# Performance work log

Measured on AMD Instinct MI355X. Metric: run time of the kernel, lower is better.

The kernel has to match this reference:

```python
import math
import jax, jax.numpy as jnp
import numpy as np

D_MODEL = 1024
N_HEAD = 16
D_K = D_MODEL // N_HEAD  # 64
D_V = D_MODEL // N_HEAD  # 64


def setup_inputs() -> dict:
    key = jax.random.key(0)
    kx, kq, kk, kv, ko = jax.random.split(key, 5)
    B, L = 4, 2048
    x = jax.random.normal(kx, (B, L, D_MODEL), dtype=jnp.float32)
    mask = jnp.zeros((B, 1, 1, L), dtype=bool)  # True = masked; all-False here
    s = 1.0 / math.sqrt(D_MODEL)
    # torch nn.Linear weights: shape (out_features, in_features), y = x @ W.T
    Wq = jax.random.normal(kq, (D_K * N_HEAD, D_MODEL), dtype=jnp.float32) * s
    Wk = jax.random.normal(kk, (D_K * N_HEAD, D_MODEL), dtype=jnp.float32) * s
    Wv = jax.random.normal(kv, (D_V * N_HEAD, D_MODEL), dtype=jnp.float32) * s
    Wo = jax.random.normal(ko, (D_MODEL, D_V * N_HEAD), dtype=jnp.float32) * s
    return {"x": x, "mask": mask, "Wq": Wq, "Wk": Wk, "Wv": Wv, "Wo": Wo}


def reference(x, mask, Wq, Wk, Wv, Wo):
    B, L, D = x.shape
    H, Dh, Dv = N_HEAD, D_K, D_V
    # projections (torch Linear: x @ W.T), then split heads -> (B,H,L,Dh)
    q = (x @ Wq.T).reshape(B, L, H, Dh).transpose(0, 2, 1, 3)
    k = (x @ Wk.T).reshape(B, L, H, Dh).transpose(0, 2, 1, 3)
    v = (x @ Wv.T).reshape(B, L, H, Dv).transpose(0, 2, 1, 3)
    scores = jnp.einsum('bhqd,bhkd->bhqk', q, k) / math.sqrt(Dh)
    scores = jnp.where(mask, -jnp.inf, scores)
    attn = jax.nn.softmax(scores, axis=-1)  # dropout p=0.0 -> identity
    out = jnp.einsum('bhqk,bhkd->bhqd', attn, v)  # (B,H,L,Dv)
    out = out.transpose(0, 2, 1, 3).reshape(B, L, H * Dv)
    return out @ Wo.T
```

## Files before the change

kernel.cpp:

```cpp
#include <hip/hip_runtime.h>

typedef __bf16 bf16_t;
typedef __bf16 bf16x4 __attribute__((ext_vector_type(4)));
typedef __bf16 bf16x8 __attribute__((ext_vector_type(8)));
typedef float f32x4 __attribute__((ext_vector_type(4)));

#define MFMA_16x16x32 __builtin_amdgcn_mfma_f32_16x16x32_bf16

#define GLD16(dst_lds, src_glb) \
  __builtin_amdgcn_global_load_lds((__attribute__((address_space(1))) void*)(void*)(src_glb), \
                                   (__attribute__((address_space(3))) void*)(dst_lds), 16, 0, 0)


__global__ void cvt_all(const float* __restrict__ x,  const float* __restrict__ wq,
                        const float* __restrict__ wk, const float* __restrict__ wv,
                        const float* __restrict__ wo,
                        bf16_t* __restrict__ xb, bf16_t* __restrict__ wqkv,
                        bf16_t* __restrict__ wob) {
    const int XN = 8 * 1024 * 1024, WN = 1024 * 1024;
    int i = (blockIdx.x * blockDim.x + threadIdx.x) * 4;
    const float* s; bf16_t* d; int off;
    if (i < XN)                { s = x;  d = xb;            off = i; }
    else if (i < XN + WN)      { s = wq; d = wqkv;          off = i - XN; }
    else if (i < XN + 2 * WN)  { s = wk; d = wqkv + WN;     off = i - XN - WN; }
    else if (i < XN + 3 * WN)  { s = wv; d = wqkv + 2 * WN; off = i - XN - 2 * WN; }
    else                       { s = wo; d = wob;           off = i - XN - 3 * WN; }
    float4 v = *(const float4*)(s + off);
    bf16x4 o;
    o[0] = (bf16_t)v.x; o[1] = (bf16_t)v.y; o[2] = (bf16_t)v.z; o[3] = (bf16_t)v.w;
    *(bf16x4*)(d + off) = o;
}

__global__ __launch_bounds__(256) void gemm_qkv(
    const bf16_t* __restrict__ A, const bf16_t* __restrict__ W,
    bf16_t* __restrict__ qo, bf16_t* __restrict__ ko, bf16_t* __restrict__ vto)
{
    constexpr int K = 1024, BK = 32;
    __shared__ bf16_t smem[16896];
    bf16_t* As = smem;
    bf16_t* Bs = smem + 4096;
    const int t = threadIdx.x;
    const int lane = t & 63, wave = t >> 6;
    const int quad = lane >> 4, l16 = lane & 15;
    const int m0 = blockIdx.x * 128, n0 = blockIdx.y * 128;
    const int wm = (wave & 1) * 64, wn = (wave >> 1) * 64;

    f32x4 acc[4][4] = {};

    const int c0 = t, c1 = t + 256;
    const int r0 = c0 >> 2, o0 = (c0 & 3) * 8;
    const int r1 = c1 >> 2, o1 = (c1 & 3) * 8;

    for (int k0 = 0; k0 < K; k0 += BK) {
        __syncthreads();
        GLD16(As + c0 * 8, A + (size_t)(m0 + r0) * K + k0 + o0);
        GLD16(As + c1 * 8, A + (size_t)(m0 + r1) * K + k0 + o1);
        GLD16(Bs + c0 * 8, W + (size_t)(n0 + r0) * K + k0 + o0);
        GLD16(Bs + c1 * 8, W + (size_t)(n0 + r1) * K + k0 + o1);
        __syncthreads();
        bf16x8 af[4], bfr[4];
#pragma unroll
        for (int i = 0; i < 4; ++i)
            af[i] = *(const bf16x8*)(As + (wm + i * 16 + l16) * BK + quad * 8);
#pragma unroll
        for (int j = 0; j < 4; ++j)
            bfr[j] = *(const bf16x8*)(Bs + (wn + j * 16 + l16) * BK + quad * 8);
#pragma unroll
        for (int i = 0; i < 4; ++i)
#pragma unroll
            for (int j = 0; j < 4; ++j)
                acc[i][j] = MFMA_16x16x32(af[i], bfr[j], acc[i][j], 0, 0, 0);
    }

    if (n0 < 2048) {
#pragma unroll
        for (int i = 0; i < 4; ++i) {
#pragma unroll
            for (int j = 0; j < 4; ++j) {
#pragma unroll
                for (int r = 0; r < 4; ++r) {
                    int row = m0 + wm + i * 16 + quad * 4 + r;
                    int col = n0 + wn + j * 16 + l16;
                    float v = acc[i][j][r];
                    int b = row >> 11, l = row & 2047;
                    int sec = col >> 10, c2 = col & 1023;
                    int h = c2 >> 6, dd = c2 & 63;
                    size_t bh = (size_t)b * 16 + h;
                    if (sec == 0) qo[(bh * 2048 + l) * 64 + dd] = (bf16_t)(v * 0.125f);
                    else          ko[(bh * 2048 + l) * 64 + dd] = (bf16_t)v;
                }
            }
        }
    } else {
        __syncthreads();
        const int hh = wave >> 1;
#pragma unroll
        for (int i = 0; i < 4; ++i) {
            int lbase = wm + (i >> 1) * 32;
            int slot0 = quad * 8 + (i & 1) * 4;
#pragma unroll
            for (int j = 0; j < 4; ++j) {
                int dd = j * 16 + l16;
                bf16x4 pk;
#pragma unroll
                for (int r = 0; r < 4; ++r) pk[r] = (bf16_t)acc[i][j][r];
                *(bf16x4*)(smem + (hh * 64 + dd) * 132 + lbase + slot0) = pk;
            }
        }
        __syncthreads();
        const int b = m0 >> 11, lb = m0 & 2047;
        const int h0 = (n0 - 2048) >> 6;
#pragma unroll
        for (int r8 = 0; r8 < 8; ++r8) {
            int c = r8 * 256 + t;
            int ch = c >> 10, cc = c & 1023;
            int dd = cc >> 4, lc = (cc & 15) * 8;
            bf16x8 vv = *(const bf16x8*)(smem + (ch * 64 + dd) * 132 + lc);
            size_t bh = (size_t)b * 16 + h0 + ch;
            *(bf16x8*)(vto + (bh * 64 + dd) * 2048 + lb + lc) = vv;
        }
    }
}

__global__ __launch_bounds__(256) void gemm_out(
    const bf16_t* __restrict__ A, const bf16_t* __restrict__ W,
    float* __restrict__ out)
{
    constexpr int K = 1024, BK = 32;
    __shared__ bf16_t As[128 * BK];
    __shared__ bf16_t Bs[128 * BK];
    const int t = threadIdx.x;
    const int lane = t & 63, wave = t >> 6;
    const int quad = lane >> 4, l16 = lane & 15;
    const int m0 = blockIdx.x * 128, n0 = blockIdx.y * 128;
    const int wm = (wave & 1) * 64, wn = (wave >> 1) * 64;

    f32x4 acc[4][4] = {};

    const int c0 = t, c1 = t + 256;
    const int r0 = c0 >> 2, o0 = (c0 & 3) * 8;
    const int r1 = c1 >> 2, o1 = (c1 & 3) * 8;

    for (int k0 = 0; k0 < K; k0 += BK) {
        __syncthreads();
        GLD16(As + c0 * 8, A + (size_t)(m0 + r0) * K + k0 + o0);
        GLD16(As + c1 * 8, A + (size_t)(m0 + r1) * K + k0 + o1);
        GLD16(Bs + c0 * 8, W + (size_t)(n0 + r0) * K + k0 + o0);
        GLD16(Bs + c1 * 8, W + (size_t)(n0 + r1) * K + k0 + o1);
        __syncthreads();
        bf16x8 af[4], bfr[4];
#pragma unroll
        for (int i = 0; i < 4; ++i)
            af[i] = *(const bf16x8*)(As + (wm + i * 16 + l16) * BK + quad * 8);
#pragma unroll
        for (int j = 0; j < 4; ++j)
            bfr[j] = *(const bf16x8*)(Bs + (wn + j * 16 + l16) * BK + quad * 8);
#pragma unroll
        for (int i = 0; i < 4; ++i)
#pragma unroll
            for (int j = 0; j < 4; ++j)
                acc[i][j] = MFMA_16x16x32(af[i], bfr[j], acc[i][j], 0, 0, 0);
    }

#pragma unroll
    for (int i = 0; i < 4; ++i)
#pragma unroll
        for (int j = 0; j < 4; ++j)
#pragma unroll
            for (int r = 0; r < 4; ++r) {
                int row = m0 + wm + i * 16 + quad * 4 + r;
                int col = n0 + wn + j * 16 + l16;
                out[(size_t)row * 1024 + col] = acc[i][j][r];
            }
}

__global__ __launch_bounds__(256, 2) void attn(
    const bf16_t* __restrict__ q, const bf16_t* __restrict__ k,
    const bf16_t* __restrict__ vt, bf16_t* __restrict__ ho)
{
    constexpr int L = 2048, DH = 64;
    const int bid = blockIdx.x;
    const int bh = bid & 63, qblk = bid >> 6;
    const bf16_t* Q   = q  + (size_t)bh * L * DH;
    const bf16_t* Kg  = k  + (size_t)bh * L * DH;
    const bf16_t* VTg = vt + (size_t)bh * L * DH;
    const int t = threadIdx.x, lane = t & 63, wave = t >> 6;
    const int quad = lane >> 4, l16 = lane & 15;
    const int qrow0 = qblk * 256 + wave * 64;

    __shared__ bf16_t Ks[4096];
    __shared__ bf16_t Vs[4096];

    const int c0 = t, c1 = t + 256;
    const bf16_t* ks0 = Kg  + (size_t)((c0 >> 2) & 63) * DH + (c0 >> 8) * 32 + (c0 & 3) * 8;
    const bf16_t* ks1 = Kg  + (size_t)((c1 >> 2) & 63) * DH + (c1 >> 8) * 32 + (c1 & 3) * 8;
    const bf16_t* vs0 = VTg + (size_t)((c0 >> 2) & 63) * L  + (c0 >> 8) * 32 + (c0 & 3) * 8;
    const bf16_t* vs1 = VTg + (size_t)((c1 >> 2) & 63) * L  + (c1 >> 8) * 32 + (c1 & 3) * 8;

    bf16x8 bq[4][2];
#pragma unroll
    for (int s4 = 0; s4 < 4; ++s4) {
        bq[s4][0] = *(const bf16x8*)(Q + (size_t)(qrow0 + s4 * 16 + l16) * DH + quad * 8);
        bq[s4][1] = *(const bf16x8*)(Q + (size_t)(qrow0 + s4 * 16 + l16) * DH + 32 + quad * 8);
    }

    f32x4 o[4][4] = {};
    float ls[4] = {};

    for (int kc = 0; kc < L; kc += 64) {
        __syncthreads();
        GLD16(Ks + c0 * 8, ks0 + (size_t)kc * DH);
        GLD16(Ks + c1 * 8, ks1 + (size_t)kc * DH);
        GLD16(Vs + c0 * 8, vs0 + kc);
        GLD16(Vs + c1 * 8, vs1 + kc);
        __syncthreads();

#pragma unroll
        for (int h = 0; h < 2; ++h) {
            bf16x8 ak[2][2];
#pragma unroll
            for (int ss = 0; ss < 2; ++ss) {
                ak[ss][0] = *(const bf16x8*)(Ks + ((h * 2 + ss) * 16 + l16) * 32 + quad * 8);
                ak[ss][1] = *(const bf16x8*)(Ks + 2048 + ((h * 2 + ss) * 16 + l16) * 32 + quad * 8);
            }
            f32x4 st[4][2];
#pragma unroll
            for (int q4 = 0; q4 < 4; ++q4)
#pragma unroll
                for (int ss = 0; ss < 2; ++ss) {
                    f32x4 z = {};
                    z = MFMA_16x16x32(ak[ss][0], bq[q4][0], z, 0, 0, 0);
                    st[q4][ss] = MFMA_16x16x32(ak[ss][1], bq[q4][1], z, 0, 0, 0);
                }
            bf16x8 p[4];
#pragma unroll
            for (int q4 = 0; q4 < 4; ++q4)
#pragma unroll
                for (int r = 0; r < 4; ++r) {
                    float e0 = __expf(st[q4][0][r]);
                    float e1 = __expf(st[q4][1][r]);
                    p[q4][r]     = (bf16_t)e0;
                    p[q4][4 + r] = (bf16_t)e1;
                    ls[q4] += e0 + e1;
                }
#pragma unroll
            for (int tt = 0; tt < 4; ++tt) {
                bf16x8 av = *(const bf16x8*)(Vs + h * 2048 + (tt * 16 + l16) * 32 + quad * 8);
#pragma unroll
                for (int q4 = 0; q4 < 4; ++q4)
                    o[q4][tt] = MFMA_16x16x32(av, p[q4], o[q4][tt], 0, 0, 0);
            }
        }
    }

    const int b = bh >> 4, hd = bh & 15;
#pragma unroll
    for (int q4 = 0; q4 < 4; ++q4) {
        float s = ls[q4];
        s += __shfl_xor(s, 16);
        s += __shfl_xor(s, 32);
        const float inv = 1.0f / s;
        const int tok = b * 2048 + qrow0 + q4 * 16 + l16;
#pragma unroll
        for (int tt = 0; tt < 4; ++tt) {
            bf16x4 ov;
#pragma unroll
            for (int r = 0; r < 4; ++r) ov[r] = (bf16_t)(o[q4][tt][r] * inv);
            *(bf16x4*)(ho + (size_t)tok * 1024 + hd * 64 + tt * 16 + quad * 4) = ov;
        }
    }
}

extern "C" void kernel_launch(void* const* d_in, const int* in_sizes, int n_in,
                              void* d_out, int out_size, void* d_ws, size_t ws_size,
                              hipStream_t stream) {
    const float* x  = (const float*)d_in[0];
    const float* Wq = (const float*)d_in[2];
    const float* Wk = (const float*)d_in[3];
    const float* Wv = (const float*)d_in[4];
    const float* Wo = (const float*)d_in[5];
    float* out = (float*)d_out;

    bf16_t* ws   = (bf16_t*)d_ws;
    bf16_t* xb   = ws;
    bf16_t* wqkv = xb   + (size_t)8192 * 1024;
    bf16_t* wob  = wqkv + (size_t)3072 * 1024;
    bf16_t* qb   = wob  + (size_t)1024 * 1024;
    bf16_t* kb   = qb   + (size_t)8192 * 1024;
    bf16_t* vtb  = kb   + (size_t)8192 * 1024;
    bf16_t* hob  = vtb  + (size_t)8192 * 1024;

    cvt_all<<<12288, 256, 0, stream>>>(x, Wq, Wk, Wv, Wo, xb, wqkv, wob);
    gemm_qkv<<<dim3(64, 24), 256, 0, stream>>>(xb, wqkv, qb, kb, vtb);
    attn<<<512, 256, 0, stream>>>(qb, kb, vtb, hob);
    gemm_out<<<dim3(64, 8), 256, 0, stream>>>(hob, wob, out);
}
```

Baseline: 258.0 us.

## Widen GEMM K-tiles with XOR-swizzled LDS and retile attention for more blocks

Both GEMMs now stage a 64-wide K slice per iteration, XOR-swizzling the LDS layout to avoid bank conflicts, which halves the number of barrier pairs. The attention kernel processes 128 keys per chunk with swizzled K/V tiles, gives each wave 32 query rows instead of 64, and launches twice as many blocks with a higher occupancy hint. The softmax scale now folds log2(e) into the Q scale so exp2f can be used. The cost is fewer query rows per wave, so K/V data loaded into LDS is reused less per block.

```diff
diff --git a/kernel.cpp b/kernel.cpp
--- a/kernel.cpp
+++ b/kernel.cpp
@@ -11,6 +11,7 @@
   __builtin_amdgcn_global_load_lds((__attribute__((address_space(1))) void*)(void*)(src_glb), \
                                    (__attribute__((address_space(3))) void*)(dst_lds), 16, 0, 0)
 
+#define QSCALE 0.18033688011112042f
 
 __global__ void cvt_all(const float* __restrict__ x,  const float* __restrict__ wq,
                         const float* __restrict__ wk, const float* __restrict__ wv,
@@ -35,10 +36,10 @@
     const bf16_t* __restrict__ A, const bf16_t* __restrict__ W,
     bf16_t* __restrict__ qo, bf16_t* __restrict__ ko, bf16_t* __restrict__ vto)
 {
-    constexpr int K = 1024, BK = 32;
+    constexpr int K = 1024, BK = 64;
     __shared__ bf16_t smem[16896];
     bf16_t* As = smem;
-    bf16_t* Bs = smem + 4096;
+    bf16_t* Bs = smem + 8192;
     const int t = threadIdx.x;
     const int lane = t & 63, wave = t >> 6;
     const int quad = lane >> 4, l16 = lane & 15;
@@ -47,29 +48,39 @@
 
     f32x4 acc[4][4] = {};
 
-    const int c0 = t, c1 = t + 256;
-    const int r0 = c0 >> 2, o0 = (c0 & 3) * 8;
-    const int r1 = c1 >> 2, o1 = (c1 & 3) * 8;
+    int goff[4];
+#pragma unroll
+    for (int m = 0; m < 4; ++m) {
+        int c = t + m * 256;
+        int row = c >> 3;
+        goff[m] = row * K + (((c & 7) ^ (row & 7)) * 8);
+    }
 
     for (int k0 = 0; k0 < K; k0 += BK) {
         __syncthreads();
-        GLD16(As + c0 * 8, A + (size_t)(m0 + r0) * K + k0 + o0);
-        GLD16(As + c1 * 8, A + (size_t)(m0 + r1) * K + k0 + o1);
-        GLD16(Bs + c0 * 8, W + (size_t)(n0 + r0) * K + k0 + o0);
-        GLD16(Bs + c1 * 8, W + (size_t)(n0 + r1) * K + k0 + o1);
-        __syncthreads();
-        bf16x8 af[4], bfr[4];
-#pragma unroll
-        for (int i = 0; i < 4; ++i)
-            af[i] = *(const bf16x8*)(As + (wm + i * 16 + l16) * BK + quad * 8);
-#pragma unroll
-        for (int j = 0; j < 4; ++j)
-            bfr[j] = *(const bf16x8*)(Bs + (wn + j * 16 + l16) * BK + quad * 8);
-#pragma unroll
-        for (int i = 0; i < 4; ++i)
+#pragma unroll
+        for (int m = 0; m < 4; ++m) {
+            int c8 = (t + m * 256) * 8;
+            GLD16(As + c8, A + (size_t)m0 * K + k0 + goff[m]);
+            GLD16(Bs + c8, W + (size_t)n0 * K + k0 + goff[m]);
+        }
+        __syncthreads();
+#pragma unroll
+        for (int half = 0; half < 2; ++half) {
+            const int sw = (((half * 4 + quad) ^ (l16 & 7)) * 8);
+            bf16x8 af[4], bfr[4];
+#pragma unroll
+            for (int i = 0; i < 4; ++i)
+                af[i] = *(const bf16x8*)(As + (wm + i * 16 + l16) * 64 + sw);
 #pragma unroll
             for (int j = 0; j < 4; ++j)
-                acc[i][j] = MFMA_16x16x32(af[i], bfr[j], acc[i][j], 0, 0, 0);
+                bfr[j] = *(const bf16x8*)(Bs + (wn + j * 16 + l16) * 64 + sw);
+#pragma unroll
+            for (int i = 0; i < 4; ++i)
+#pragma unroll
+                for (int j = 0; j < 4; ++j)
+                    acc[i][j] = MFMA_16x16x32(af[i], bfr[j], acc[i][j], 0, 0, 0);
+        }
     }
 
     if (n0 < 2048) {
@@ -86,7 +97,7 @@
                     int sec = col >> 10, c2 = col & 1023;
                     int h = c2 >> 6, dd = c2 & 63;
                     size_t bh = (size_t)b * 16 + h;
-                    if (sec == 0) qo[(bh * 2048 + l) * 64 + dd] = (bf16_t)(v * 0.125f);
+                    if (sec == 0) qo[(bh * 2048 + l) * 64 + dd] = (bf16_t)(v * QSCALE);
                     else          ko[(bh * 2048 + l) * 64 + dd] = (bf16_t)v;
                 }
             }
@@ -126,9 +137,10 @@
     const bf16_t* __restrict__ A, const bf16_t* __restrict__ W,
     float* __restrict__ out)
 {
-    constexpr int K = 1024, BK = 32;
-    __shared__ bf16_t As[128 * BK];
-    __shared__ bf16_t Bs[128 * BK];
+    constexpr int K = 1024, BK = 64;
+    __shared__ bf16_t smem[16384];
+    bf16_t* As = smem;
+    bf16_t* Bs = smem + 8192;
     const int t = threadIdx.x;
     const int lane = t & 63, wave = t >> 6;
     const int quad = lane >> 4, l16 = lane & 15;
@@ -137,29 +149,39 @@
 
     f32x4 acc[4][4] = {};
 
-    const int c0 = t, c1 = t + 256;
-    const int r0 = c0 >> 2, o0 = (c0 & 3) * 8;
-    const int r1 = c1 >> 2, o1 = (c1 & 3) * 8;
+    int goff[4];
+#pragma unroll
+    for (int m = 0; m < 4; ++m) {
+        int c = t + m * 256;
+        int row = c >> 3;
+        goff[m] = row * K + (((c & 7) ^ (row & 7)) * 8);
+    }
 
     for (int k0 = 0; k0 < K; k0 += BK) {
         __syncthreads();
-        GLD16(As + c0 * 8, A + (size_t)(m0 + r0) * K + k0 + o0);
-        GLD16(As + c1 * 8, A + (size_t)(m0 + r1) * K + k0 + o1);
-        GLD16(Bs + c0 * 8, W + (size_t)(n0 + r0) * K + k0 + o0);
-        GLD16(Bs + c1 * 8, W + (size_t)(n0 + r1) * K + k0 + o1);
-        __syncthreads();
-        bf16x8 af[4], bfr[4];
-#pragma unroll
-        for (int i = 0; i < 4; ++i)
-            af[i] = *(const bf16x8*)(As + (wm + i * 16 + l16) * BK + quad * 8);
-#pragma unroll
-        for (int j = 0; j < 4; ++j)
-            bfr[j] = *(const bf16x8*)(Bs + (wn + j * 16 + l16) * BK + quad * 8);
-#pragma unroll
-        for (int i = 0; i < 4; ++i)
+#pragma unroll
+        for (int m = 0; m < 4; ++m) {
+            int c8 = (t + m * 256) * 8;
+            GLD16(As + c8, A + (size_t)m0 * K + k0 + goff[m]);
+            GLD16(Bs + c8, W + (size_t)n0 * K + k0 + goff[m]);
+        }
+        __syncthreads();
+#pragma unroll
+        for (int half = 0; half < 2; ++half) {
+            const int sw = (((half * 4 + quad) ^ (l16 & 7)) * 8);
+            bf16x8 af[4], bfr[4];
+#pragma unroll
+            for (int i = 0; i < 4; ++i)
+                af[i] = *(const bf16x8*)(As + (wm + i * 16 + l16) * 64 + sw);
 #pragma unroll
             for (int j = 0; j < 4; ++j)
-                acc[i][j] = MFMA_16x16x32(af[i], bfr[j], acc[i][j], 0, 0, 0);
+                bfr[j] = *(const bf16x8*)(Bs + (wn + j * 16 + l16) * 64 + sw);
+#pragma unroll
+            for (int i = 0; i < 4; ++i)
+#pragma unroll
+                for (int j = 0; j < 4; ++j)
+                    acc[i][j] = MFMA_16x16x32(af[i], bfr[j], acc[i][j], 0, 0, 0);
+        }
     }
 
 #pragma unroll
@@ -174,7 +196,7 @@
             }
 }
 
-__global__ __launch_bounds__(256, 2) void attn(
+__global__ __launch_bounds__(256, 4) void attn(
     const bf16_t* __restrict__ q, const bf16_t* __restrict__ k,
     const bf16_t* __restrict__ vt, bf16_t* __restrict__ ho)
 {
@@ -186,86 +208,89 @@
     const bf16_t* VTg = vt + (size_t)bh * L * DH;
     const int t = threadIdx.x, lane = t & 63, wave = t >> 6;
     const int quad = lane >> 4, l16 = lane & 15;
-    const int qrow0 = qblk * 256 + wave * 64;
-
-    __shared__ bf16_t Ks[4096];
-    __shared__ bf16_t Vs[4096];
-
-    const int c0 = t, c1 = t + 256;
-    const bf16_t* ks0 = Kg  + (size_t)((c0 >> 2) & 63) * DH + (c0 >> 8) * 32 + (c0 & 3) * 8;
-    const bf16_t* ks1 = Kg  + (size_t)((c1 >> 2) & 63) * DH + (c1 >> 8) * 32 + (c1 & 3) * 8;
-    const bf16_t* vs0 = VTg + (size_t)((c0 >> 2) & 63) * L  + (c0 >> 8) * 32 + (c0 & 3) * 8;
-    const bf16_t* vs1 = VTg + (size_t)((c1 >> 2) & 63) * L  + (c1 >> 8) * 32 + (c1 & 3) * 8;
-
-    bf16x8 bq[4][2];
-#pragma unroll
-    for (int s4 = 0; s4 < 4; ++s4) {
-        bq[s4][0] = *(const bf16x8*)(Q + (size_t)(qrow0 + s4 * 16 + l16) * DH + quad * 8);
-        bq[s4][1] = *(const bf16x8*)(Q + (size_t)(qrow0 + s4 * 16 + l16) * DH + 32 + quad * 8);
-    }
-
-    f32x4 o[4][4] = {};
-    float ls[4] = {};
-
-    for (int kc = 0; kc < L; kc += 64) {
-        __syncthreads();
-        GLD16(Ks + c0 * 8, ks0 + (size_t)kc * DH);
-        GLD16(Ks + c1 * 8, ks1 + (size_t)kc * DH);
-        GLD16(Vs + c0 * 8, vs0 + kc);
-        GLD16(Vs + c1 * 8, vs1 + kc);
-        __syncthreads();
-
-#pragma unroll
-        for (int h = 0; h < 2; ++h) {
+    const int qrow0 = qblk * 128 + wave * 32;
+
+    __shared__ bf16_t Ks[8192];
+    __shared__ bf16_t Vs[8192];
+
+    int koff[4], voff[4];
+#pragma unroll
+    for (int m = 0; m < 4; ++m) {
+        int c = t + m * 256;
+        int key = (c >> 2) & 127, pl = c >> 9;
+        koff[m] = key * DH + pl * 32 + (((c & 3) ^ (key & 3)) * 8);
+        int dv = (c >> 2) & 63, kpl = (c >> 8) & 3;
+        voff[m] = dv * L + kpl * 32 + (((c & 3) ^ (dv & 3)) * 8);
+    }
+
+    bf16x8 bq[2][2];
+#pragma unroll
+    for (int qs = 0; qs < 2; ++qs) {
+        bq[qs][0] = *(const bf16x8*)(Q + (size_t)(qrow0 + qs * 16 + l16) * DH + quad * 8);
+        bq[qs][1] = *(const bf16x8*)(Q + (size_t)(qrow0 + qs * 16 + l16) * DH + 32 + quad * 8);
+    }
+
+    f32x4 o[2][4] = {};
+    float ls[2] = {};
+    const int swl = (quad ^ (l16 & 3)) * 8;
+
+    for (int kc = 0; kc < L; kc += 128) {
+        __syncthreads();
+#pragma unroll
+        for (int m = 0; m < 4; ++m) {
+            int c8 = (t + m * 256) * 8;
+            GLD16(Ks + c8, Kg + (size_t)kc * DH + koff[m]);
+            GLD16(Vs + c8, VTg + kc + voff[m]);
+        }
+        __syncthreads();
+
+#pragma unroll
+        for (int g = 0; g < 4; ++g) {
             bf16x8 ak[2][2];
 #pragma unroll
             for (int ss = 0; ss < 2; ++ss) {
-                ak[ss][0] = *(const bf16x8*)(Ks + ((h * 2 + ss) * 16 + l16) * 32 + quad * 8);
-                ak[ss][1] = *(const bf16x8*)(Ks + 2048 + ((h * 2 + ss) * 16 + l16) * 32 + quad * 8);
-            }
-            f32x4 st[4][2];
-#pragma unroll
-            for (int q4 = 0; q4 < 4; ++q4)
-#pragma unroll
-                for (int ss = 0; ss < 2; ++ss) {
-                    f32x4 z = {};
-                    z = MFMA_16x16x32(ak[ss][0], bq[q4][0], z, 0, 0, 0);
-                    st[q4][ss] = MFMA_16x16x32(ak[ss][1], bq[q4][1], z, 0, 0, 0);
+                ak[ss][0] = *(const bf16x8*)(Ks + (g * 32 + ss * 16 + l16) * 32 + swl);
+                ak[ss][1] = *(const bf16x8*)(Ks + 4096 + (g * 32 + ss * 16 + l16) * 32 + swl);
+            }
+            bf16x8 p[2];
+#pragma unroll
+            for (int qs = 0; qs < 2; ++qs) {
+                f32x4 st0 = {}, st1 = {};
+                st0 = MFMA_16x16x32(ak[0][0], bq[qs][0], st0, 0, 0, 0);
+                st0 = MFMA_16x16x32(ak[0][1], bq[qs][1], st0, 0, 0, 0);
+                st1 = MFMA_16x16x32(ak[1][0], bq[qs][0], st1, 0, 0, 0);
+                st1 = MFMA_16x16x32(ak[1][1], bq[qs][1], st1, 0, 0, 0);
+#pragma unroll
+                for (int r = 0; r < 4; ++r) {
+                    float e0 = exp2f(st0[r]);
+                    float e1 = exp2f(st1[r]);
+                    p[qs][r]     = (bf16_t)e0;
+                    p[qs][4 + r] = (bf16_t)e1;
+                    ls[qs] += e0 + e1;
                 }
-            bf16x8 p[4];
-#pragma unroll
-            for (int q4 = 0; q4 < 4; ++q4)
-#pragma unroll
-                for (int r = 0; r < 4; ++r) {
-                    float e0 = __expf(st[q4][0][r]);
-                    float e1 = __expf(st[q4][1][r]);
-                    p[q4][r]     = (bf16_t)e0;
-                    p[q4][4 + r] = (bf16_t)e1;
-                    ls[q4] += e0 + e1;
-                }
+            }
 #pragma unroll
             for (int tt = 0; tt < 4; ++tt) {
-                bf16x8 av = *(const bf16x8*)(Vs + h * 2048 + (tt * 16 + l16) * 32 + quad * 8);
-#pragma unroll
-                for (int q4 = 0; q4 < 4; ++q4)
-                    o[q4][tt] = MFMA_16x16x32(av, p[q4], o[q4][tt], 0, 0, 0);
+                bf16x8 av = *(const bf16x8*)(Vs + g * 2048 + (tt * 16 + l16) * 32 + swl);
+                o[0][tt] = MFMA_16x16x32(av, p[0], o[0][tt], 0, 0, 0);
+                o[1][tt] = MFMA_16x16x32(av, p[1], o[1][tt], 0, 0, 0);
             }
         }
     }
 
     const int b = bh >> 4, hd = bh & 15;
 #pragma unroll
-    for (int q4 = 0; q4 < 4; ++q4) {
-        float s = ls[q4];
+    for (int qs = 0; qs < 2; ++qs) {
+        float s = ls[qs];
         s += __shfl_xor(s, 16);
         s += __shfl_xor(s, 32);
         const float inv = 1.0f / s;
-        const int tok = b * 2048 + qrow0 + q4 * 16 + l16;
+        const int tok = b * 2048 + qrow0 + qs * 16 + l16;
 #pragma unroll
         for (int tt = 0; tt < 4; ++tt) {
             bf16x4 ov;
 #pragma unroll
-            for (int r = 0; r < 4; ++r) ov[r] = (bf16_t)(o[q4][tt][r] * inv);
+            for (int r = 0; r < 4; ++r) ov[r] = (bf16_t)(o[qs][tt][r] * inv);
             *(bf16x4*)(ho + (size_t)tok * 1024 + hd * 64 + tt * 16 + quad * 4) = ov;
         }
     }
@@ -292,6 +317,6 @@
 
     cvt_all<<<12288, 256, 0, stream>>>(x, Wq, Wk, Wv, Wo, xb, wqkv, wob);
     gemm_qkv<<<dim3(64, 24), 256, 0, stream>>>(xb, wqkv, qb, kb, vtb);
-    attn<<<512, 256, 0, stream>>>(qb, kb, vtb, hob);
+    attn<<<1024, 256, 0, stream>>>(qb, kb, vtb, hob);
     gemm_out<<<dim3(64, 8), 256, 0, stream>>>(hob, wob, out);
 }
```

Measured after the change: 285.5 us. 1.11x slower.
